# Kernel tuning notes

Measured on AMD Instinct MI355X. Metric: run time of the kernel, lower is better.

Reference implementation:

```python
import jax, jax.numpy as jnp
import numpy as np

H = 256; DS = 8; DC = 4; DI = 512; DTR = 16; NH = 4; EPS = 1e-5
B, N, F, E, S, LC = 8, 512, 32, 8192, 512, 8


def setup_inputs() -> dict:
    key = jax.random.key(0)
    ks = iter(jax.random.split(key, 64))
    def rn(shape, s=0.05):
        return jax.random.normal(next(ks), shape, jnp.float32) * s
    z = lambda *s: jnp.zeros(s, jnp.float32)
    inp = dict(
        node_features=jax.random.normal(next(ks), (B, N, F), jnp.float32),
        edge_index=jax.random.randint(next(ks), (B, 2, E), 0, N),
        W_init=rn((F, H)), b_init=z(H),
        gcn1_W=rn((H, H)), gcn1_b=z(H),
        gcn2_W=rn((H, H)), gcn2_b=z(H),
        in_proj_W=rn((H, 2 * DI)),
        conv_W=rn((DI, DC)), conv_b=z(DI),
        xproj_W=rn((DI, DTR + 2 * DS)),
        dt_W=rn((DTR, DI)), dt_b=z(DI),
        A_log=jnp.log(jnp.tile(jnp.arange(1, DS + 1, dtype=jnp.float32), (DI, 1))),
        Dp=jnp.ones((DI,), jnp.float32),
        out_W=rn((DI, H)),
        Wq=rn((H, H)), bq=z(H), Wk=rn((H, H)), bk=z(H), Wv=rn((H, H)), bv=z(H),
        Wo=rn((H, H)), bo=z(H),
        fus_W=rn((3 * H, H)), fus_b=z(H),
        ln_g=jnp.ones((H,), jnp.float32), ln_b=z(H),
        cw=rn((H, 1)), cb=z(1), hw=rn((H, 4)), hb=z(4), tw=rn((H, 3)), tb=z(3),
        p1w=rn((H, S)), p1b=z(S), p2w=rn((H, S)), p2b=z(S),
        dw=rn((H, S)), db=z(S), sw=rn((H, LC)), sb=z(LC))
    return inp


def gcn(x, src, dst, W, b):
    # PyG GCNConv: self-loops + symmetric deg^{-1/2} normalization, scatter-add.
    n = x.shape[0]
    loops = jnp.arange(n)
    s = jnp.concatenate([src, loops]); d = jnp.concatenate([dst, loops])
    deg = jax.ops.segment_sum(jnp.ones_like(d, x.dtype), d, n)
    dinv = jnp.where(deg > 0, jax.lax.rsqrt(deg), 0.0)
    norm = (dinv[s] * dinv[d])[:, None]
    m = x @ W
    return jax.ops.segment_sum(m[s] * norm, d, n) + b


def mamba(x, in_W, conv_W, conv_b, xproj_W, dt_W, dt_b, A_log, Dp, out_W):
    # mamba_ssm Mamba block, batch=1, seq len L = total nodes.
    L = x.shape[0]
    xz = x @ in_W
    xc, zg = xz[:, :DI], xz[:, DI:]
    xp = jnp.pad(xc, ((DC - 1, 0), (0, 0)))            # causal depthwise conv
    win = xp[jnp.arange(L)[:, None] + jnp.arange(DC)[None, :]]  # [L,K,DI]
    xc = jax.nn.silu(jnp.einsum('lkd,dk->ld', win, conv_W) + conv_b)
    proj = xc @ xproj_W
    dt, Bm, Cm = proj[:, :DTR], proj[:, DTR:DTR + DS], proj[:, DTR + DS:]
    delta = jax.nn.softplus(dt @ dt_W + dt_b)           # [L,DI]
    A = -jnp.exp(A_log)                                 # [DI,DS]
    dA = jnp.exp(delta[:, :, None] * A[None])           # [L,DI,DS]
    dBx = delta[:, :, None] * Bm[:, None, :] * xc[:, :, None]
    def step(h, inp):
        dA_t, dBx_t, C_t = inp
        h = dA_t * h + dBx_t
        return h, (h * C_t[None, :]).sum(-1)
    _, y = jax.lax.scan(step, jnp.zeros((DI, DS), x.dtype), (dA, dBx, Cm))
    y = (y + Dp * xc) * jax.nn.silu(zg)
    return y @ out_W


def mha(x, Wq, bq, Wk, bk, Wv, bv, Wo, bo):
    L = x.shape[0]; hd = H // NH
    q = (x @ Wq + bq).reshape(L, NH, hd)
    k = (x @ Wk + bk).reshape(L, NH, hd)
    v = (x @ Wv + bv).reshape(L, NH, hd)
    s = jnp.einsum('qhd,khd->hqk', q, k) / np.float32(np.sqrt(hd))
    a = jax.nn.softmax(s, axis=-1)
    o = jnp.einsum('hqk,khd->qhd', a, v).reshape(L, H)
    return o @ Wo + bo


def _forward(node_features, edge_index, W_init, b_init, gcn1_W, gcn1_b, gcn2_W, gcn2_b,
             in_proj_W, conv_W, conv_b, xproj_W, dt_W, dt_b, A_log, Dp, out_W,
             Wq, bq, Wk, bk, Wv, bv, Wo, bo, fus_W, fus_b, ln_g, ln_b,
             cw, cb, hw, hb, tw, tb, p1w, p1b, p2w, p2b, dw, db, sw, sb):
    Bsz, Nn, Ff = node_features.shape
    x = node_features.reshape(Bsz * Nn, Ff)
    # offset per-graph edge indices into the flat node space (batching loop)
    ei = (edge_index + (jnp.arange(Bsz) * Nn)[:, None, None]).transpose(1, 0, 2).reshape(2, -1)
    src, dst = ei[0], ei[1]
    h = jax.nn.relu(x @ W_init + b_init)
    h = jax.nn.relu(gcn(h, src, dst, gcn1_W, gcn1_b))
    h = jax.nn.relu(gcn(h, src, dst, gcn2_W, gcn2_b))
    m = mamba(h, in_proj_W, conv_W, conv_b, xproj_W, dt_W, dt_b, A_log, Dp, out_W)
    a = mha(h, Wq, bq, Wk, bk, Wv, bv, Wo, bo)
    fused = jax.nn.relu(jnp.concatenate([h, m, a], -1) @ fus_W + fus_b)
    res = fused + h
    mu = res.mean(-1, keepdims=True)
    var = ((res - mu) ** 2).mean(-1, keepdims=True)
    hf = (res - mu) * jax.lax.rsqrt(var + EPS) * ln_g + ln_b
    batch = jnp.repeat(jnp.arange(Bsz), Nn)
    pooled = jax.ops.segment_sum(hf, batch, Bsz) / jnp.float32(Nn)  # global_mean_pool
    outs = [pooled @ cw + cb, pooled @ hw + hb, pooled @ tw + tb,
            pooled @ p1w + p1b, pooled @ p2w + p2b, pooled @ dw + db,
            pooled @ sw + sb]
    return jnp.concatenate(outs, -1)  # [B, 1+4+3+S+S+S+LC]


def reference(node_features, edge_index, W_init, b_init, gcn1_W, gcn1_b, gcn2_W, gcn2_b,
              in_proj_W, conv_W, conv_b, xproj_W, dt_W, dt_b, A_log, Dp, out_W,
              Wq, bq, Wk, bk, Wv, bv, Wo, bo, fus_W, fus_b, ln_g, ln_b,
              cw, cb, hw, hb, tw, tb, p1w, p1b, p2w, p2b, dw, db, sw, sb):
    return _forward(node_features, edge_index, W_init, b_init, gcn1_W, gcn1_b, gcn2_W, gcn2_b,
                    in_proj_W, conv_W, conv_b, xproj_W, dt_W, dt_b, A_log, Dp, out_W,
                    Wq, bq, Wk, bk, Wv, bv, Wo, bo, fus_W, fus_b, ln_g, ln_b,
                    cw, cb, hw, hb, tw, tb, p1w, p1b, p2w, p2b, dw, db, sw, sb)
```

## Files before the change

kernel.cpp:

```cpp
#include <hip/hip_runtime.h>
#include <hip/hip_bf16.h>
#include <math.h>

typedef __hip_bfloat16 hbf;
typedef short bf16x8 __attribute__((ext_vector_type(8)));
typedef float f32x4 __attribute__((ext_vector_type(4)));

constexpr int NL  = 4096;
constexpr int HH  = 256;
constexpr int NE  = 8192;
constexpr int DIc = 512;
constexpr int DSc = 8;
constexpr int CLc = 16;
constexpr int NOUT = 12416;

constexpr size_t O_MBUF  = 0;
constexpr size_t O_QK    = 1048576;
constexpr size_t O_H2    = 2097152;
constexpr size_t O_CATB  = 3145728;
constexpr size_t O_XZB   = 4718592;
constexpr size_t O_XC    = 6815744;
constexpr size_t O_DELTA = 8912896;
constexpr size_t O_PROJ  = 11010048;
constexpr size_t O_HST   = 11141120;
constexpr size_t O_Y     = 12189696;
constexpr size_t O_POOL  = 13238272;
constexpr size_t O_DINV  = 13240320;
constexpr size_t O_B768  = 13244416;
constexpr size_t O_INT   = 13245184;
constexpr size_t O_WT    = 13327112;
constexpr size_t O_XB    = 13839112;
constexpr size_t O_H0B   = 13904648;
constexpr size_t O_H2B   = 14428936;
constexpr size_t O_XCB   = 14953224;
constexpr size_t O_DTAB  = 16001800;
constexpr size_t O_QKB   = 16067584;
constexpr size_t O_VTB   = 17116160;
constexpr size_t O_PART  = 17640448;
constexpr size_t O_HWT   = 17902592;

constexpr int NW = 12;
__device__ __constant__ int wc_cum[NW+1] = {
    0, 8192, 73728, 139264, 155648, 172032, 303104, 565248,
    630784, 696320, 761856, 827392, 1024000 };
__device__ __constant__ int wc_K [NW] = {32,256,256,512,16,512,256,256,256,256,256,768};
__device__ __constant__ int wc_N [NW] = {256,256,256,32,512,256,1024,256,256,256,256,256};
__device__ __constant__ int wc_Kp[NW] = {32,256,256,512,32,512,256,256,256,256,256,768};
struct WSrc { const float* p[NW]; };
struct HSrc { const float* p[7]; };
struct OPtrs { hbf* p[8]; };

__device__ __constant__ int hw_b[8]  = {0,1,5,8,520,1032,1544,1552};
__device__ __constant__ int hw_nc[7] = {1,4,3,512,512,512,8};

constexpr int PR_W = 1024000;
constexpr int PR_X = PR_W + 131072;
constexpr int PR_B = PR_X + 768;
constexpr int PR_P = PR_B + 262144;
constexpr int PR_I = PR_P + 4096;
constexpr int PR_H = PR_I + 397312;
__global__ __launch_bounds__(256) void prep_k(WSrc ws, hbf* __restrict__ wt,
        const float* __restrict__ x, hbf* __restrict__ xb,
        const float* __restrict__ bq, const float* __restrict__ bk,
        const float* __restrict__ bv,
        float* __restrict__ b768, float* __restrict__ part, int* __restrict__ cnt,
        HSrc hs, hbf* __restrict__ hwt) {
    int idx = blockIdx.x*256 + threadIdx.x;
    if (idx < PR_W) {
        int lo = 0, hi = NW-1;
        while (lo < hi) { int mid = (lo+hi+1)>>1; if (idx >= wc_cum[mid]) lo = mid; else hi = mid-1; }
        int local = idx - wc_cum[lo];
        int Kp = wc_Kp[lo], K = wc_K[lo], N = wc_N[lo];
        int n = local / Kp, k = local - n*Kp;
        float v = (k < K) ? ws.p[lo][(size_t)k*N + n] : 0.0f;
        wt[idx] = __float2bfloat16(v);
    } else if (idx < PR_X) {
        int i = idx - PR_W;
        xb[i] = __float2bfloat16(x[i]);
    } else if (idx < PR_B) {
        int i = idx - PR_X;
        b768[i] = (i < 256) ? bq[i] : (i < 512 ? bk[i-256] : bv[i-512]);
    } else if (idx < PR_P) {
        part[idx - PR_B] = 0.0f;
    } else if (idx < PR_I) {
        cnt[idx - PR_P] = 0;
    } else if (idx < PR_H) {
        int i = idx - PR_I;
        int j = i >> 8, k = i & 255;
        int seg = 0;
        while (j >= hw_b[seg+1]) seg++;
        int col = j - hw_b[seg], nc = hw_nc[seg];
        hwt[(size_t)j*256 + k] = __float2bfloat16(hs.p[seg][(size_t)k*nc + col]);
    }
}

__global__ void bucket_k(const int* __restrict__ ei, int* __restrict__ cnt,
                         int* __restrict__ csr) {
    int i = blockIdx.x*256 + threadIdx.x;
    int b = i >> 13, e = i & 8191;
    int src = ei[b*2*NE + e]      + (b << 9);
    int dst = ei[b*2*NE + NE + e] + (b << 9);
    int slot = atomicAdd(&cnt[dst], 1);
    if (slot < 64) csr[(dst << 6) + slot] = src;
}

__global__ __launch_bounds__(256) void gather_k(const hbf* __restrict__ m,
                        const int* __restrict__ csr, const int* __restrict__ cnt,
                        hbf* __restrict__ outb) {
    int n = blockIdx.x, c = threadIdx.x;
    int cn = min(cnt[n], 64);
    float dn = rsqrtf(1.0f + (float)cn);
    float acc = __bfloat162float(m[(size_t)n*HH + c]) * dn * dn;
    for (int e = 0; e < cn; e++) {
        int s = csr[(n << 6) + e];
        float ds = rsqrtf(1.0f + (float)min(cnt[s], 64));
        acc += __bfloat162float(m[(size_t)s*HH + c]) * (ds * dn);
    }
    outb[(size_t)n*HH + c] = __float2bfloat16(acc);
}

template<int ACT, int OUTM>
__global__ __launch_bounds__(512) void mg_k(const unsigned short* __restrict__ A,
        const unsigned short* __restrict__ Bt, const float* __restrict__ bias,
        void* __restrict__ Cp, int ldc, void* __restrict__ Cp2, void* __restrict__ Cp3,
        const float* __restrict__ resid, int ldr, int M, int K, int N)
{
    __shared__ __align__(16) unsigned short Asm[2][64][40];
    __shared__ __align__(16) unsigned short Bsm[2][64][40];
    int t = threadIdx.x;
    int lane = t & 63, w = t >> 6;
    int wm = w & 3, wn = w >> 2;
    int row0 = blockIdx.x * 64, col0 = blockIdx.y * 64;
    int sr = t >> 3;
    int sk8 = (t & 7) * 8;
    int su = sk8 >> 5, so = sk8 & 31;
    f32x4 acc0 = {}, acc1 = {};
    int fr = lane & 15, fq8 = (lane >> 4) * 8;

    uint4 zz = make_uint4(0u,0u,0u,0u);
    uint4 ra = zz, rb = zz;
    bool bnv = (col0 + sr) < N;
    if (sk8 < K) {
        ra = *(const uint4*)&A[(size_t)(row0+sr)*K + sk8];
        if (bnv) rb = *(const uint4*)&Bt[(size_t)(col0+sr)*K + sk8];
    }

    for (int k0 = 0; k0 < K; k0 += 64) {
        __syncthreads();
        *(uint4*)&Asm[su][sr][so] = ra;
        *(uint4*)&Bsm[su][sr][so] = rb;
        __syncthreads();
        int kn = k0 + 64;
        if (kn < K) {
            ra = rb = zz;
            if (kn + sk8 < K) {
                ra = *(const uint4*)&A[(size_t)(row0+sr)*K + kn + sk8];
                if (bnv) rb = *(const uint4*)&Bt[(size_t)(col0+sr)*K + kn + sk8];
            }
        }
        #pragma unroll
        for (int ks = 0; ks < 2; ks++) {
            bf16x8 a  = *(bf16x8*)&Asm[ks][wm*16 + fr][fq8];
            bf16x8 b0 = *(bf16x8*)&Bsm[ks][wn*32 + fr][fq8];
            bf16x8 b1 = *(bf16x8*)&Bsm[ks][wn*32 + 16 + fr][fq8];
            acc0 = __builtin_amdgcn_mfma_f32_16x16x32_bf16(a, b0, acc0, 0, 0, 0);
            acc1 = __builtin_amdgcn_mfma_f32_16x16x32_bf16(a, b1, acc1, 0, 0, 0);
        }
    }

    int fc = lane & 15, frq = (lane >> 4) * 4;
    if constexpr (OUTM == 4) {
        #pragma unroll
        for (int nt = 0; nt < 2; nt++) {
            int col = col0 + wn*32 + nt*16 + fc;
            if (col >= 32) continue;
            f32x4& av = nt ? acc1 : acc0;
            #pragma unroll
            for (int i = 0; i < 4; i++) {
                int row = row0 + wm*16 + frq + i;
                float v = av[i];
                ((float*)Cp)[(size_t)row*32 + col] = v;
                ((hbf*)Cp2)[(size_t)row*32 + col] = __float2bfloat16((col < 16) ? v : 0.0f);
            }
        }
    } else if constexpr (OUTM == 5) {
        if (col0 < 1024) {
            #pragma unroll
            for (int nt = 0; nt < 2; nt++) {
                int col = col0 + wn*32 + nt*16 + fc;
                f32x4& av = nt ? acc1 : acc0;
                #pragma unroll
                for (int i = 0; i < 4; i++) {
                    int row = row0 + wm*16 + frq + i;
                    ((hbf*)Cp)[(size_t)row*1024 + col] = __float2bfloat16(av[i]);
                }
            }
        } else if (col0 < 1536) {
            #pragma unroll
            for (int nt = 0; nt < 2; nt++) {
                int gcol = col0 + wn*32 + nt*16 + fc;
                int col = gcol - 1024;
                float bvv = bias[col];
                float sc = (col < 256) ? 0.125f : 1.0f;
                f32x4& av = nt ? acc1 : acc0;
                #pragma unroll
                for (int i = 0; i < 4; i++) {
                    int row = row0 + wm*16 + frq + i;
                    ((hbf*)Cp2)[(size_t)row*512 + col] = __float2bfloat16((av[i] + bvv) * sc);
                }
            }
        } else {
            __shared__ __align__(16) unsigned short Ts[64][72];
            #pragma unroll
            for (int nt = 0; nt < 2; nt++) {
                int gcol = col0 + wn*32 + nt*16 + fc;
                float bvv = bias[gcol - 1024];
                f32x4& av = nt ? acc1 : acc0;
                #pragma unroll
                for (int i = 0; i < 4; i++)
                    *(hbf*)&Ts[wn*32 + nt*16 + fc][wm*16 + frq + i] = __float2bfloat16(av[i] + bvv);
            }
            __syncthreads();
            int c = t >> 3, rs = (t & 7) * 8;
            *(uint4*)((hbf*)Cp3 + (size_t)(col0 - 1536 + c)*NL + row0 + rs) = *(uint4*)&Ts[c][rs];
        }
    } else if constexpr (OUTM == 6) {
        #pragma unroll
        for (int nt = 0; nt < 2; nt++) {
            int col = col0 + wn*32 + nt*16 + fc;
            float bvv = bias[col];
            f32x4& av = nt ? acc1 : acc0;
            #pragma unroll
            for (int i = 0; i < 4; i++) {
                int row = row0 + wm*16 + frq + i;
                float v = fmaxf(av[i] + bvv, 0.0f);
                ((float*)Cp)[(size_t)row*HH + col] = v;
                hbf hv = __float2bfloat16(v);
                ((hbf*)Cp2)[(size_t)row*HH + col] = hv;
                ((hbf*)Cp3)[(size_t)row*768 + col] = hv;
            }
        }
    } else {
        #pragma unroll
        for (int nt = 0; nt < 2; nt++) {
            int col = col0 + wn*32 + nt*16 + fc;
            if (col >= N) continue;
            float bvv = bias ? bias[col] : 0.0f;
            f32x4& av = nt ? acc1 : acc0;
            #pragma unroll
            for (int i = 0; i < 4; i++) {
                int row = row0 + wm*16 + frq + i;
                float v = av[i] + bvv;
                if (ACT == 1) v = fmaxf(v, 0.0f);
                if (ACT == 2) v = (v > 20.0f) ? v : log1pf(expf(v));
                if (resid) v += resid[(size_t)row*ldr + col];
                if (OUTM == 0) ((float*)Cp)[(size_t)row*ldc + col] = v;
                else           ((hbf*)Cp)[(size_t)row*ldc + col] = __float2bfloat16(v);
            }
        }
    }
}

__global__ __launch_bounds__(256) void conv_k(const hbf* __restrict__ xzb,
                       const float* __restrict__ cW,
                       const float* __restrict__ cb, hbf* __restrict__ xcb) {
    int i = blockIdx.x*256 + threadIdx.x;
    int l = i >> 6, d8 = (i & 63) << 3;
    float acc[8];
    {
        float4 c0 = *(const float4*)&cb[d8];
        float4 c1 = *(const float4*)&cb[d8+4];
        acc[0]=c0.x; acc[1]=c0.y; acc[2]=c0.z; acc[3]=c0.w;
        acc[4]=c1.x; acc[5]=c1.y; acc[6]=c1.z; acc[7]=c1.w;
    }
    float4 cw4[8];
    #pragma unroll
    for (int j = 0; j < 8; j++) cw4[j] = *(const float4*)&cW[(d8+j)*4];
    #pragma unroll
    for (int k = 0; k < 4; k++) {
        int ls = l - 3 + k;
        if (ls < 0) continue;
        bf16x8 v = *(const bf16x8*)&xzb[(size_t)ls*1024 + d8];
        #pragma unroll
        for (int j = 0; j < 8; j++) {
            short tv = v[j]; hbf hv; *(short*)&hv = tv;
            float wk = (k == 0) ? cw4[j].x : (k == 1) ? cw4[j].y : (k == 2) ? cw4[j].z : cw4[j].w;
            acc[j] += __bfloat162float(hv) * wk;
        }
    }
    hbf out[8];
    #pragma unroll
    for (int j = 0; j < 8; j++) {
        float r = acc[j] / (1.0f + __expf(-acc[j]));
        out[j] = __float2bfloat16(r);
    }
    *(uint4*)&xcb[(size_t)l*512 + d8] = *(uint4*)out;
}

__global__ __launch_bounds__(256) void scan1_k(const float* __restrict__ delta,
                        const hbf* __restrict__ xc, const float* __restrict__ proj,
                        const float* __restrict__ Alog,
                        float* __restrict__ P, float* __restrict__ Hl)
{
    int c = blockIdx.x >> 1;
    int d = ((blockIdx.x & 1) << 8) + threadIdx.x;
    float Ac[DSc], pr[DSc], h[DSc];
    #pragma unroll
    for (int s2 = 0; s2 < DSc; s2++) { Ac[s2] = -__expf(Alog[d*DSc+s2]); pr[s2]=1.0f; h[s2]=0.0f; }
    int l0 = c * CLc;
    for (int l = l0; l < l0 + CLc; l++) {
        float dl = delta[(size_t)l*DIc + d];
        float dx = dl * __bfloat162float(xc[(size_t)l*DIc + d]);
        const float* pb = proj + l*32 + 16;
        #pragma unroll
        for (int s2 = 0; s2 < DSc; s2++) {
            float a = __expf(dl * Ac[s2]);
            h[s2] = a*h[s2] + dx*pb[s2];
            pr[s2] *= a;
        }
    }
    #pragma unroll
    for (int s2 = 0; s2 < DSc; s2++) {
        P [(size_t)(c*DSc+s2)*DIc + d] = pr[s2];
        Hl[(size_t)(c*DSc+s2)*DIc + d] = h[s2];
    }
}

__global__ __launch_bounds__(256) void scan2t_k(const float* __restrict__ P,
                        const float* __restrict__ Hl, float* __restrict__ Hst) {
    __shared__ float Ps[256][17], Hs[256][17];
    int t = threadIdx.x, sg = blockIdx.x;
    int si = t & 15, cb = t >> 4;
    #pragma unroll
    for (int it = 0; it < 16; it++) {
        int c = it*16 + cb;
        size_t off = (size_t)c*4096 + sg*16 + si;
        Ps[c][si] = P[off];
        Hs[c][si] = Hl[off];
    }
    __syncthreads();
    int si2 = t >> 4, g = t & 15;
    int lane = t & 63;
    float Pg = 1.0f, Hg = 0.0f;
    #pragma unroll
    for (int j = 0; j < 16; j++) {
        int c = g*16 + j;
        float pc = Ps[c][si2], hc = Hs[c][si2];
        Hg = hc + pc*Hg;
        Pg = pc*Pg;
    }
    #pragma unroll
    for (int off = 1; off < 16; off <<= 1) {
        float Pp = __shfl(Pg, lane - off);
        float Hp = __shfl(Hg, lane - off);
        if (g >= off) { Hg = Hg + Pg*Hp; Pg = Pg*Pp; }
    }
    float carry = __shfl(Hg, lane - 1);
    if (g == 0) carry = 0.0f;
    float h = carry;
    #pragma unroll
    for (int j = 0; j < 16; j++) {
        int c = g*16 + j;
        float pc = Ps[c][si2], hc = Hs[c][si2];
        Hs[c][si2] = h;
        h = hc + pc*h;
    }
    __syncthreads();
    #pragma unroll
    for (int it = 0; it < 16; it++) {
        int c = it*16 + cb;
        Hst[(size_t)c*4096 + sg*16 + si] = Hs[c][si];
    }
}

__global__ __launch_bounds__(256) void scan3_k(const float* __restrict__ delta,
                        const hbf* __restrict__ xc, const float* __restrict__ proj,
                        const float* __restrict__ Alog, const float* __restrict__ Hst,
                        const float* __restrict__ Dp, const hbf* __restrict__ xzb,
                        hbf* __restrict__ Y)
{
    int c = blockIdx.x >> 1;
    int d = ((blockIdx.x & 1) << 8) + threadIdx.x;
    float Ac[DSc], h[DSc];
    #pragma unroll
    for (int s2 = 0; s2 < DSc; s2++) {
        Ac[s2] = -__expf(Alog[d*DSc+s2]);
        h[s2]  = Hst[(size_t)(c*DSc+s2)*DIc + d];
    }
    float dpv = Dp[d];
    int l0 = c * CLc;
    for (int l = l0; l < l0 + CLc; l++) {
        float dl = delta[(size_t)l*DIc + d];
        float xv = __bfloat162float(xc[(size_t)l*DIc + d]);
        float dx = dl * xv;
        const float* pb = proj + l*32 + 16;
        float y = 0.0f;
        #pragma unroll
        for (int s2 = 0; s2 < DSc; s2++) {
            float a = __expf(dl * Ac[s2]);
            h[s2] = a*h[s2] + dx*pb[s2];
            y += h[s2] * pb[8+s2];
        }
        float z = __bfloat162float(xzb[(size_t)l*1024 + 512 + d]);
        float sz = z / (1.0f + __expf(-z));
        Y[(size_t)l*DIc + d] = __float2bfloat16((y + dpv*xv) * sz);
    }
}

__global__ __launch_bounds__(512, 8) void attn_part_k(const unsigned short* __restrict__ QK,
                       const unsigned short* __restrict__ Vt,
                       OPtrs op, float* __restrict__ lsum)
{
    __shared__ __align__(16) unsigned short QPs[128][72];
    __shared__ __align__(16) unsigned short Ks[64][72];
    __shared__ __align__(16) unsigned short Vs[64][72];
    int t = threadIdx.x, lane = t & 63, w = t >> 6;
    int h = blockIdx.y, q0 = blockIdx.x * 128, skc = blockIdx.z;
    int fm = lane & 15, fq = lane >> 4;

    {
        int qr = t >> 2, qc = (t & 3) * 16;
        const unsigned short* src = &QK[(size_t)(q0+qr)*512 + h*64 + qc];
        *(uint4*)&QPs[qr][qc]     = *(const uint4*)&src[0];
        *(uint4*)&QPs[qr][qc + 8] = *(const uint4*)&src[8];
    }
    __syncthreads();
    bf16x8 qa[2];
    #pragma unroll
    for (int ks = 0; ks < 2; ks++)
        qa[ks] = *(bf16x8*)&QPs[w*16 + fm][ks*32 + fq*8];

    bf16x8 ones;
    #pragma unroll
    for (int j = 0; j < 8; j++) ones[j] = (short)0x3F80;

    f32x4 o[4] = {};
    f32x4 ol = {};
    int sr = t >> 3, sk = (t & 7) * 8;
    const unsigned short* Kb = QK + 256;
    int kt = skc * 512;
    uint4 ka = *(const uint4*)&Kb[(size_t)(kt+sr)*512 + h*64 + sk];
    uint4 va = *(const uint4*)&Vt[(size_t)(h*64+sr)*NL + kt + sk];

    for (int it = 0; it < 8; it++) {
        __syncthreads();
        *(uint4*)&Ks[sr][sk] = ka;
        *(uint4*)&Vs[sr][sk] = va;
        __syncthreads();
        if (it < 7) {
            int kn = kt + 64;
            ka = *(const uint4*)&Kb[(size_t)(kn+sr)*512 + h*64 + sk];
            va = *(const uint4*)&Vt[(size_t)(h*64+sr)*NL + kn + sk];
        }
        #pragma unroll
        for (int np = 0; np < 2; np++) {
            f32x4 s0 = {}, s1 = {};
            __builtin_amdgcn_s_setprio(1);
            #pragma unroll
            for (int ks = 0; ks < 2; ks++) {
                bf16x8 kb0 = *(bf16x8*)&Ks[(np*2+0)*16 + fm][ks*32 + fq*8];
                bf16x8 kb1 = *(bf16x8*)&Ks[(np*2+1)*16 + fm][ks*32 + fq*8];
                s0 = __builtin_amdgcn_mfma_f32_16x16x32_bf16(qa[ks], kb0, s0, 0, 0, 0);
                s1 = __builtin_amdgcn_mfma_f32_16x16x32_bf16(qa[ks], kb1, s1, 0, 0, 0);
            }
            __builtin_amdgcn_s_setprio(0);
            #pragma unroll
            for (int i = 0; i < 4; i++) {
                float p0 = __expf(s0[i] - 4.0f);
                float p1 = __expf(s1[i] - 4.0f);
                *(hbf*)&QPs[w*16 + fq*4 + i][(np*2+0)*16 + fm] = __float2bfloat16(p0);
                *(hbf*)&QPs[w*16 + fq*4 + i][(np*2+1)*16 + fm] = __float2bfloat16(p1);
            }
        }
        __builtin_amdgcn_s_setprio(1);
        #pragma unroll
        for (int ks = 0; ks < 2; ks++) {
            bf16x8 pa = *(bf16x8*)&QPs[w*16 + fm][ks*32 + fq*8];
            #pragma unroll
            for (int nt = 0; nt < 4; nt++) {
                bf16x8 vb = *(bf16x8*)&Vs[nt*16 + fm][ks*32 + fq*8];
                o[nt] = __builtin_amdgcn_mfma_f32_16x16x32_bf16(pa, vb, o[nt], 0, 0, 0);
            }
            ol = __builtin_amdgcn_mfma_f32_16x16x32_bf16(pa, ones, ol, 0, 0, 0);
        }
        __builtin_amdgcn_s_setprio(0);
        kt += 64;
    }
    hbf* Op = op.p[skc];
    #pragma unroll
    for (int i = 0; i < 4; i++) {
        int row = w*16 + fq*4 + i;
        #pragma unroll
        for (int nt = 0; nt < 4; nt++)
            Op[(size_t)(q0 + row)*HH + h*64 + nt*16 + fm] = __float2bfloat16(o[nt][i]);
    }
    if (fm == 0) {
        #pragma unroll
        for (int i = 0; i < 4; i++)
            lsum[(size_t)(skc*4 + h)*NL + q0 + w*16 + fq*4 + i] = ol[i];
    }
}

__global__ __launch_bounds__(256) void amerge_k(OPtrs op, const float* __restrict__ lsum,
                                                hbf* __restrict__ aob) {
    int row = blockIdx.x, t = threadIdx.x, h = t >> 6;
    float L = 0.0f, s = 0.0f;
    #pragma unroll
    for (int c = 0; c < 8; c++) {
        L += lsum[(size_t)(c*4 + h)*NL + row];
        s += __bfloat162float(op.p[c][(size_t)row*HH + t]);
    }
    aob[(size_t)row*HH + t] = __float2bfloat16(s / L);
}

__global__ __launch_bounds__(256) void ln_k(const float* __restrict__ X,
                    const float* __restrict__ g, const float* __restrict__ b,
                    float* __restrict__ part) {
    __shared__ float red[4];
    int r = blockIdx.x, t = threadIdx.x;
    float v = X[(size_t)r*HH + t];
    float s = v;
    #pragma unroll
    for (int o = 32; o > 0; o >>= 1) s += __shfl_down(s, o);
    if ((t & 63) == 0) red[t >> 6] = s;
    __syncthreads();
    float mean = (red[0]+red[1]+red[2]+red[3]) * (1.0f/256.0f);
    float dfv = v - mean;
    float s2 = dfv*dfv;
    #pragma unroll
    for (int o = 32; o > 0; o >>= 1) s2 += __shfl_down(s2, o);
    __syncthreads();
    if ((t & 63) == 0) red[t >> 6] = s2;
    __syncthreads();
    float var = (red[0]+red[1]+red[2]+red[3]) * (1.0f/256.0f);
    float y = dfv * rsqrtf(var + 1e-5f) * g[t] + b[t];
    atomicAdd(&part[(size_t)(r & 127)*2048 + (r >> 9)*HH + t], y * (1.0f/512.0f));
}

__global__ void reduce_k(const float* __restrict__ part, float* __restrict__ pooled) {
    int i = blockIdx.x*256 + threadIdx.x;
    float s = 0.0f;
    #pragma unroll 8
    for (int p = 0; p < 128; p++) s += part[(size_t)p*2048 + i];
    pooled[i] = s;
}

__global__ __launch_bounds__(256) void heads_k(const float* __restrict__ pooled,
        const hbf* __restrict__ hwt,
        const float* cbh, const float* hb, const float* tb, const float* p1b,
        const float* p2b, const float* db, const float* sb, float* __restrict__ out)
{
    int idx = blockIdx.x*4 + (threadIdx.x >> 6);
    int lane = threadIdx.x & 63;
    if (idx >= NOUT) return;
    int b = idx / 1552, j = idx - b*1552;
    const float* bi; int col;
    if (j < 1)         { bi = cbh; col = j;        }
    else if (j < 5)    { bi = hb;  col = j - 1;    }
    else if (j < 8)    { bi = tb;  col = j - 5;    }
    else if (j < 520)  { bi = p1b; col = j - 8;    }
    else if (j < 1032) { bi = p2b; col = j - 520;  }
    else if (j < 1544) { bi = db;  col = j - 1032; }
    else               { bi = sb;  col = j - 1544; }
    const float* pl = pooled + b*HH;
    const hbf* wr = hwt + (size_t)j*256;
    int k4 = lane * 4;
    float4 pv = *(const float4*)&pl[k4];
    short4 wv = *(const short4*)&wr[k4];
    hbf w0, w1, w2, w3;
    *(short*)&w0 = wv.x; *(short*)&w1 = wv.y; *(short*)&w2 = wv.z; *(short*)&w3 = wv.w;
    float s = pv.x*__bfloat162float(w0) + pv.y*__bfloat162float(w1)
            + pv.z*__bfloat162float(w2) + pv.w*__bfloat162float(w3);
    #pragma unroll
    for (int o = 32; o > 0; o >>= 1) s += __shfl_down(s, o);
    if (lane == 0) out[idx] = s + bi[col];
}

extern "C" void kernel_launch(void* const* d_in, const int* in_sizes, int n_in,
                              void* d_out, int out_size, void* d_ws, size_t ws_size,
                              hipStream_t stream)
{
    (void)in_sizes; (void)n_in; (void)out_size; (void)ws_size;
    const float* x      = (const float*)d_in[0];
    const int*   ei     = (const int*)  d_in[1];
    const float* W_init = (const float*)d_in[2];
    const float* b_init = (const float*)d_in[3];
    const float* g1W = (const float*)d_in[4];
    const float* g1b = (const float*)d_in[5];
    const float* g2W = (const float*)d_in[6];
    const float* g2b = (const float*)d_in[7];
    const float* inW = (const float*)d_in[8];
    const float* cW  = (const float*)d_in[9];
    const float* cb  = (const float*)d_in[10];
    const float* xpW = (const float*)d_in[11];
    const float* dtW = (const float*)d_in[12];
    const float* dtb = (const float*)d_in[13];
    const float* Alog= (const float*)d_in[14];
    const float* Dp  = (const float*)d_in[15];
    const float* outW= (const float*)d_in[16];
    const float* Wq  = (const float*)d_in[17];
    const float* bq  = (const float*)d_in[18];
    const float* Wk  = (const float*)d_in[19];
    const float* bk  = (const float*)d_in[20];
    const float* Wv  = (const float*)d_in[21];
    const float* bv  = (const float*)d_in[22];
    const float* Wo  = (const float*)d_in[23];
    const float* bo  = (const float*)d_in[24];
    const float* fusW= (const float*)d_in[25];
    const float* fusb= (const float*)d_in[26];
    const float* lng = (const float*)d_in[27];
    const float* lnb = (const float*)d_in[28];
    const float* cwp = (const float*)d_in[29];
    const float* cbp = (const float*)d_in[30];
    const float* hwp = (const float*)d_in[31];
    const float* hbp = (const float*)d_in[32];
    const float* twp = (const float*)d_in[33];
    const float* tbp = (const float*)d_in[34];
    const float* p1w = (const float*)d_in[35];
    const float* p1b = (const float*)d_in[36];
    const float* p2w = (const float*)d_in[37];
    const float* p2b = (const float*)d_in[38];
    const float* dwp = (const float*)d_in[39];
    const float* dbp = (const float*)d_in[40];
    const float* swp = (const float*)d_in[41];
    const float* sbp = (const float*)d_in[42];

    float* fw = (float*)d_ws;
    int* iw = (int*)(fw + O_INT);
    int* cnt = iw;
    int* csr = (int*)(fw + O_XC);

    hbf* wt   = (hbf*)(fw + O_WT);
    hbf* xb   = (hbf*)(fw + O_XB);
    hbf* h0b  = (hbf*)(fw + O_H0B);
    hbf* h2b  = (hbf*)(fw + O_H2B);
    hbf* xcb  = (hbf*)(fw + O_XCB);
    hbf* dtab = (hbf*)(fw + O_DTAB);
    hbf* xzb  = (hbf*)(fw + O_XZB);
    hbf* yb   = (hbf*)(fw + O_Y);
    hbf* aob  = (hbf*)(fw + O_Y);
    hbf* catb = (hbf*)(fw + O_CATB);
    hbf* qkB  = (hbf*)(fw + O_QKB);
    hbf* vtB  = (hbf*)(fw + O_VTB);
    hbf* aggb = (hbf*)(fw + O_MBUF);
    float* fused = fw + O_XC;
    float* b768 = fw + O_B768;
    float* part = fw + O_PART;
    hbf* hwt  = (hbf*)(fw + O_HWT);

    float* scanP  = fw + O_MBUF;
    float* scanHl = fw + O_QK;
    float* scanHst= fw + O_HST;
    float* lsum   = fw + O_HST;

    OPtrs op;
    op.p[0] = (hbf*)(fw + O_MBUF);
    op.p[1] = (hbf*)(fw + O_MBUF + 524288);
    op.p[2] = (hbf*)(fw + O_DELTA);
    op.p[3] = (hbf*)(fw + O_DELTA + 524288);
    op.p[4] = (hbf*)(fw + O_DELTA + 1048576);
    op.p[5] = (hbf*)(fw + O_DELTA + 1572864);
    op.p[6] = (hbf*)(fw + O_XZB);
    op.p[7] = (hbf*)(fw + O_XZB + 524288);

    hbf* WtInit  = wt + 0;
    hbf* WtG1    = wt + 8192;
    hbf* WtG2    = wt + 73728;
    hbf* WtXp    = wt + 139264;
    hbf* WtDt    = wt + 155648;
    hbf* WtOut   = wt + 172032;
    hbf* WtInQKV = wt + 303104;
    hbf* WtO     = wt + 761856;
    hbf* WtFus   = wt + 827392;

    WSrc wsrc;
    wsrc.p[0]=W_init; wsrc.p[1]=g1W; wsrc.p[2]=g2W; wsrc.p[3]=xpW; wsrc.p[4]=dtW;
    wsrc.p[5]=outW; wsrc.p[6]=inW; wsrc.p[7]=Wq; wsrc.p[8]=Wk; wsrc.p[9]=Wv;
    wsrc.p[10]=Wo; wsrc.p[11]=fusW;
    HSrc hsrc;
    hsrc.p[0]=cwp; hsrc.p[1]=hwp; hsrc.p[2]=twp; hsrc.p[3]=p1w;
    hsrc.p[4]=p2w; hsrc.p[5]=dwp; hsrc.p[6]=swp;
    prep_k<<<(PR_H+255)/256,256,0,stream>>>(wsrc, wt, x, xb, bq, bk, bv, b768,
                                            part, cnt, hsrc, hwt);

    bucket_k<<<256,256,0,stream>>>(ei, cnt, csr);

    mg_k<1,1><<<dim3(64,4),512,0,stream>>>((const unsigned short*)xb, (const unsigned short*)WtInit,
        b_init, h0b, 256, nullptr, nullptr, nullptr, 0, NL, 32, 256);
    gather_k<<<4096,256,0,stream>>>(h0b, csr, cnt, aggb);
    mg_k<1,1><<<dim3(64,4),512,0,stream>>>((const unsigned short*)aggb, (const unsigned short*)WtG1,
        g1b, h0b, 256, nullptr, nullptr, nullptr, 0, NL, 256, 256);
    gather_k<<<4096,256,0,stream>>>(h0b, csr, cnt, aggb);
    mg_k<1,6><<<dim3(64,4),512,0,stream>>>((const unsigned short*)aggb, (const unsigned short*)WtG2,
        g2b, fw+O_H2, 256, h2b, catb, nullptr, 0, NL, 256, 256);

    mg_k<0,5><<<dim3(64,28),512,0,stream>>>((const unsigned short*)h2b, (const unsigned short*)WtInQKV,
        b768, xzb, 1024, qkB, vtB, nullptr, 0, NL, 256, 1792);

    conv_k<<<1024,256,0,stream>>>(xzb, cW, cb, xcb);
    mg_k<0,4><<<dim3(64,1),512,0,stream>>>((const unsigned short*)xcb, (const unsigned short*)WtXp,
        nullptr, fw+O_PROJ, 32, dtab, nullptr, nullptr, 0, NL, 512, 32);
    mg_k<2,0><<<dim3(64,8),512,0,stream>>>((const unsigned short*)dtab, (const unsigned short*)WtDt,
        dtb, fw+O_DELTA, 512, nullptr, nullptr, nullptr, 0, NL, 32, 512);
    scan1_k<<<512,256,0,stream>>>(fw+O_DELTA, xcb, fw+O_PROJ, Alog, scanP, scanHl);
    scan2t_k<<<256,256,0,stream>>>(scanP, scanHl, scanHst);
    scan3_k<<<512,256,0,stream>>>(fw+O_DELTA, xcb, fw+O_PROJ, Alog, scanHst, Dp, xzb, yb);
    mg_k<0,1><<<dim3(64,4),512,0,stream>>>((const unsigned short*)yb, (const unsigned short*)WtOut,
        nullptr, catb + 256, 768, nullptr, nullptr, nullptr, 0, NL, 512, 256);

    attn_part_k<<<dim3(32,4,8),512,0,stream>>>((const unsigned short*)qkB,
        (const unsigned short*)vtB, op, lsum);
    amerge_k<<<4096,256,0,stream>>>(op, lsum, aob);
    mg_k<0,1><<<dim3(64,4),512,0,stream>>>((const unsigned short*)aob, (const unsigned short*)WtO,
        bo, catb + 512, 768, nullptr, nullptr, nullptr, 0, NL, 256, 256);

    mg_k<1,0><<<dim3(64,4),512,0,stream>>>((const unsigned short*)catb, (const unsigned short*)WtFus,
        fusb, fused, 256, nullptr, nullptr, fw+O_H2, 256, NL, 768, 256);
    ln_k<<<4096,256,0,stream>>>(fused, lng, lnb, part);
    reduce_k<<<8,256,0,stream>>>(part, fw+O_POOL);
    heads_k<<<(NOUT+3)/4,256,0,stream>>>(fw+O_POOL, hwt, cbp,hbp,tbp,p1b,p2b,dbp,sbp,
                                         (float*)d_out);
}
```

Before: 352.5 us.

## Shrink GEMM tiles to 32x32 for more blocks; vectorize attention merge

The bf16 MFMA GEMM kernel moves from 64x64 tiles with 512 threads to 32x32 tiles with 256 threads, so each wave computes a single 16x16 tile. Every GEMM launch gets four times as many blocks, which fills more of the GPU's compute units for these small M=4096 problems. In exchange, each block reuses loaded data less and the B-column bounds check is dropped. The attention merge kernel now has each thread handle 8 contiguous bf16 values with vector loads and stores, 8 rows per block, instead of one element per thread.

```diff
diff --git a/kernel.cpp b/kernel.cpp
--- a/kernel.cpp
+++ b/kernel.cpp
@@ -120,137 +120,110 @@
 }
 
 template<int ACT, int OUTM>
-__global__ __launch_bounds__(512) void mg_k(const unsigned short* __restrict__ A,
+__global__ __launch_bounds__(256) void mg_k(const unsigned short* __restrict__ A,
         const unsigned short* __restrict__ Bt, const float* __restrict__ bias,
         void* __restrict__ Cp, int ldc, void* __restrict__ Cp2, void* __restrict__ Cp3,
         const float* __restrict__ resid, int ldr, int M, int K, int N)
 {
-    __shared__ __align__(16) unsigned short Asm[2][64][40];
-    __shared__ __align__(16) unsigned short Bsm[2][64][40];
+    __shared__ __align__(16) unsigned short Asm[2][32][40];
+    __shared__ __align__(16) unsigned short Bsm[2][32][40];
     int t = threadIdx.x;
     int lane = t & 63, w = t >> 6;
-    int wm = w & 3, wn = w >> 2;
-    int row0 = blockIdx.x * 64, col0 = blockIdx.y * 64;
-    int sr = t >> 3;
-    int sk8 = (t & 7) * 8;
-    int su = sk8 >> 5, so = sk8 & 31;
-    f32x4 acc0 = {}, acc1 = {};
+    int wr = (w & 1) * 16, wc = (w >> 1) * 16;
+    int row0 = blockIdx.x * 32, col0 = blockIdx.y * 32;
+    int sr = t >> 3, sk8 = (t & 7) * 8;
+    f32x4 acc = {};
     int fr = lane & 15, fq8 = (lane >> 4) * 8;
 
     uint4 zz = make_uint4(0u,0u,0u,0u);
     uint4 ra = zz, rb = zz;
-    bool bnv = (col0 + sr) < N;
     if (sk8 < K) {
         ra = *(const uint4*)&A[(size_t)(row0+sr)*K + sk8];
-        if (bnv) rb = *(const uint4*)&Bt[(size_t)(col0+sr)*K + sk8];
+        rb = *(const uint4*)&Bt[(size_t)(col0+sr)*K + sk8];
     }
 
     for (int k0 = 0; k0 < K; k0 += 64) {
         __syncthreads();
-        *(uint4*)&Asm[su][sr][so] = ra;
-        *(uint4*)&Bsm[su][sr][so] = rb;
+        *(uint4*)&Asm[sk8>>5][sr][sk8 & 31] = ra;
+        *(uint4*)&Bsm[sk8>>5][sr][sk8 & 31] = rb;
         __syncthreads();
         int kn = k0 + 64;
         if (kn < K) {
             ra = rb = zz;
             if (kn + sk8 < K) {
                 ra = *(const uint4*)&A[(size_t)(row0+sr)*K + kn + sk8];
-                if (bnv) rb = *(const uint4*)&Bt[(size_t)(col0+sr)*K + kn + sk8];
+                rb = *(const uint4*)&Bt[(size_t)(col0+sr)*K + kn + sk8];
             }
         }
         #pragma unroll
         for (int ks = 0; ks < 2; ks++) {
-            bf16x8 a  = *(bf16x8*)&Asm[ks][wm*16 + fr][fq8];
-            bf16x8 b0 = *(bf16x8*)&Bsm[ks][wn*32 + fr][fq8];
-            bf16x8 b1 = *(bf16x8*)&Bsm[ks][wn*32 + 16 + fr][fq8];
-            acc0 = __builtin_amdgcn_mfma_f32_16x16x32_bf16(a, b0, acc0, 0, 0, 0);
-            acc1 = __builtin_amdgcn_mfma_f32_16x16x32_bf16(a, b1, acc1, 0, 0, 0);
+            bf16x8 a = *(bf16x8*)&Asm[ks][wr + fr][fq8];
+            bf16x8 b = *(bf16x8*)&Bsm[ks][wc + fr][fq8];
+            acc = __builtin_amdgcn_mfma_f32_16x16x32_bf16(a, b, acc, 0, 0, 0);
         }
     }
 
     int fc = lane & 15, frq = (lane >> 4) * 4;
     if constexpr (OUTM == 4) {
-        #pragma unroll
-        for (int nt = 0; nt < 2; nt++) {
-            int col = col0 + wn*32 + nt*16 + fc;
-            if (col >= 32) continue;
-            f32x4& av = nt ? acc1 : acc0;
+        int col = wc + fc;
+        #pragma unroll
+        for (int i = 0; i < 4; i++) {
+            int row = row0 + wr + frq + i;
+            float v = acc[i];
+            ((float*)Cp)[(size_t)row*32 + col] = v;
+            ((hbf*)Cp2)[(size_t)row*32 + col] = __float2bfloat16((col < 16) ? v : 0.0f);
+        }
+    } else if constexpr (OUTM == 5) {
+        if (col0 < 1024) {
+            int col = col0 + wc + fc;
             #pragma unroll
             for (int i = 0; i < 4; i++) {
-                int row = row0 + wm*16 + frq + i;
-                float v = av[i];
-                ((float*)Cp)[(size_t)row*32 + col] = v;
-                ((hbf*)Cp2)[(size_t)row*32 + col] = __float2bfloat16((col < 16) ? v : 0.0f);
-            }
-        }
-    } else if constexpr (OUTM == 5) {
-        if (col0 < 1024) {
-            #pragma unroll
-            for (int nt = 0; nt < 2; nt++) {
-                int col = col0 + wn*32 + nt*16 + fc;
-                f32x4& av = nt ? acc1 : acc0;
-                #pragma unroll
-                for (int i = 0; i < 4; i++) {
-                    int row = row0 + wm*16 + frq + i;
-                    ((hbf*)Cp)[(size_t)row*1024 + col] = __float2bfloat16(av[i]);
-                }
+                int row = row0 + wr + frq + i;
+                ((hbf*)Cp)[(size_t)row*1024 + col] = __float2bfloat16(acc[i]);
             }
         } else if (col0 < 1536) {
+            int gcol = col0 + wc + fc;
+            int col = gcol - 1024;
+            float bvv = bias[col];
+            float sc = (col < 256) ? 0.125f : 1.0f;
             #pragma unroll
-            for (int nt = 0; nt < 2; nt++) {
-                int gcol = col0 + wn*32 + nt*16 + fc;
-                int col = gcol - 1024;
-                float bvv = bias[col];
-                float sc = (col < 256) ? 0.125f : 1.0f;
-                f32x4& av = nt ? acc1 : acc0;
-                #pragma unroll
-                for (int i = 0; i < 4; i++) {
-                    int row = row0 + wm*16 + frq + i;
-                    ((hbf*)Cp2)[(size_t)row*512 + col] = __float2bfloat16((av[i] + bvv) * sc);
-                }
+            for (int i = 0; i < 4; i++) {
+                int row = row0 + wr + frq + i;
+                ((hbf*)Cp2)[(size_t)row*512 + col] = __float2bfloat16((acc[i] + bvv) * sc);
             }
         } else {
-            __shared__ __align__(16) unsigned short Ts[64][72];
+            __shared__ __align__(16) unsigned short Ts[32][48];
+            int gcol = col0 + wc + fc;
+            float bvv = bias[gcol - 1024];
             #pragma unroll
-            for (int nt = 0; nt < 2; nt++) {
-                int gcol = col0 + wn*32 + nt*16 + fc;
-                float bvv = bias[gcol - 1024];
-                f32x4& av = nt ? acc1 : acc0;
-                #pragma unroll
-                for (int i = 0; i < 4; i++)
-                    *(hbf*)&Ts[wn*32 + nt*16 + fc][wm*16 + frq + i] = __float2bfloat16(av[i] + bvv);
+            for (int i = 0; i < 4; i++)
+                *(hbf*)&Ts[wc + fc][wr + frq + i] = __float2bfloat16(acc[i] + bvv);
+            __syncthreads();
+            if (t < 128) {
+                int c = t >> 2, rs = (t & 3) * 8;
+                *(uint4*)((hbf*)Cp3 + (size_t)(col0 - 1536 + c)*NL + row0 + rs) = *(uint4*)&Ts[c][rs];
             }
-            __syncthreads();
-            int c = t >> 3, rs = (t & 7) * 8;
-            *(uint4*)((hbf*)Cp3 + (size_t)(col0 - 1536 + c)*NL + row0 + rs) = *(uint4*)&Ts[c][rs];
         }
     } else if constexpr (OUTM == 6) {
-        #pragma unroll
-        for (int nt = 0; nt < 2; nt++) {
-            int col = col0 + wn*32 + nt*16 + fc;
-            float bvv = bias[col];
-            f32x4& av = nt ? acc1 : acc0;
+        int col = col0 + wc + fc;
+        float bvv = bias[col];
+        #pragma unroll
+        for (int i = 0; i < 4; i++) {
+            int row = row0 + wr + frq + i;
+            float v = fmaxf(acc[i] + bvv, 0.0f);
+            ((float*)Cp)[(size_t)row*HH + col] = v;
+            hbf hv = __float2bfloat16(v);
+            ((hbf*)Cp2)[(size_t)row*HH + col] = hv;
+            ((hbf*)Cp3)[(size_t)row*768 + col] = hv;
+        }
+    } else {
+        int col = col0 + wc + fc;
+        if (col < N) {
+            float bvv = bias ? bias[col] : 0.0f;
             #pragma unroll
             for (int i = 0; i < 4; i++) {
-                int row = row0 + wm*16 + frq + i;
-                float v = fmaxf(av[i] + bvv, 0.0f);
-                ((float*)Cp)[(size_t)row*HH + col] = v;
-                hbf hv = __float2bfloat16(v);
-                ((hbf*)Cp2)[(size_t)row*HH + col] = hv;
-                ((hbf*)Cp3)[(size_t)row*768 + col] = hv;
-            }
-        }
-    } else {
-        #pragma unroll
-        for (int nt = 0; nt < 2; nt++) {
-            int col = col0 + wn*32 + nt*16 + fc;
-            if (col >= N) continue;
-            float bvv = bias ? bias[col] : 0.0f;
-            f32x4& av = nt ? acc1 : acc0;
-            #pragma unroll
-            for (int i = 0; i < 4; i++) {
-                int row = row0 + wm*16 + frq + i;
-                float v = av[i] + bvv;
+                int row = row0 + wr + frq + i;
+                float v = acc[i] + bvv;
                 if (ACT == 1) v = fmaxf(v, 0.0f);
                 if (ACT == 2) v = (v > 20.0f) ? v : log1pf(expf(v));
                 if (resid) v += resid[(size_t)row*ldr + col];
@@ -503,14 +476,28 @@
 
 __global__ __launch_bounds__(256) void amerge_k(OPtrs op, const float* __restrict__ lsum,
                                                 hbf* __restrict__ aob) {
-    int row = blockIdx.x, t = threadIdx.x, h = t >> 6;
-    float L = 0.0f, s = 0.0f;
+    int t = threadIdx.x;
+    int row = blockIdx.x*8 + (t >> 5);
+    int d8 = (t & 31) << 3;
+    int h = d8 >> 6;
+    float L = 0.0f;
+    #pragma unroll
+    for (int c = 0; c < 8; c++) L += lsum[(size_t)(c*4 + h)*NL + row];
+    float inv = 1.0f / L;
+    float s[8] = {};
     #pragma unroll
     for (int c = 0; c < 8; c++) {
-        L += lsum[(size_t)(c*4 + h)*NL + row];
-        s += __bfloat162float(op.p[c][(size_t)row*HH + t]);
-    }
-    aob[(size_t)row*HH + t] = __float2bfloat16(s / L);
+        bf16x8 v = *(const bf16x8*)&op.p[c][(size_t)row*HH + d8];
+        #pragma unroll
+        for (int j = 0; j < 8; j++) {
+            short tv = v[j]; hbf hv; *(short*)&hv = tv;
+            s[j] += __bfloat162float(hv);
+        }
+    }
+    hbf out[8];
+    #pragma unroll
+    for (int j = 0; j < 8; j++) out[j] = __float2bfloat16(s[j] * inv);
+    *(uint4*)&aob[(size_t)row*HH + d8] = *(uint4*)out;
 }
 
 __global__ __launch_bounds__(256) void ln_k(const float* __restrict__ X,
@@ -685,36 +672,36 @@
 
     bucket_k<<<256,256,0,stream>>>(ei, cnt, csr);
 
-    mg_k<1,1><<<dim3(64,4),512,0,stream>>>((const unsigned short*)xb, (const unsigned short*)WtInit,
+    mg_k<1,1><<<dim3(128,8),256,0,stream>>>((const unsigned short*)xb, (const unsigned short*)WtInit,
         b_init, h0b, 256, nullptr, nullptr, nullptr, 0, NL, 32, 256);
     gather_k<<<4096,256,0,stream>>>(h0b, csr, cnt, aggb);
-    mg_k<1,1><<<dim3(64,4),512,0,stream>>>((const unsigned short*)aggb, (const unsigned short*)WtG1,
+    mg_k<1,1><<<dim3(128,8),256,0,stream>>>((const unsigned short*)aggb, (const unsigned short*)WtG1,
         g1b, h0b, 256, nullptr, nullptr, nullptr, 0, NL, 256, 256);
     gather_k<<<4096,256,0,stream>>>(h0b, csr, cnt, aggb);
-    mg_k<1,6><<<dim3(64,4),512,0,stream>>>((const unsigned short*)aggb, (const unsigned short*)WtG2,
+    mg_k<1,6><<<dim3(128,8),256,0,stream>>>((const unsigned short*)aggb, (const unsigned short*)WtG2,
         g2b, fw+O_H2, 256, h2b, catb, nullptr, 0, NL, 256, 256);
 
-    mg_k<0,5><<<dim3(64,28),512,0,stream>>>((const unsigned short*)h2b, (const unsigned short*)WtInQKV,
+    mg_k<0,5><<<dim3(128,56),256,0,stream>>>((const unsigned short*)h2b, (const unsigned short*)WtInQKV,
         b768, xzb, 1024, qkB, vtB, nullptr, 0, NL, 256, 1792);
 
     conv_k<<<1024,256,0,stream>>>(xzb, cW, cb, xcb);
-    mg_k<0,4><<<dim3(64,1),512,0,stream>>>((const unsigned short*)xcb, (const unsigned short*)WtXp,
+    mg_k<0,4><<<dim3(128,1),256,0,stream>>>((const unsigned short*)xcb, (const unsigned short*)WtXp,
         nullptr, fw+O_PROJ, 32, dtab, nullptr, nullptr, 0, NL, 512, 32);
-    mg_k<2,0><<<dim3(64,8),512,0,stream>>>((const unsigned short*)dtab, (const unsigned short*)WtDt,
+    mg_k<2,0><<<dim3(128,16),256,0,stream>>>((const unsigned short*)dtab, (const unsigned short*)WtDt,
         dtb, fw+O_DELTA, 512, nullptr, nullptr, nullptr, 0, NL, 32, 512);
     scan1_k<<<512,256,0,stream>>>(fw+O_DELTA, xcb, fw+O_PROJ, Alog, scanP, scanHl);
     scan2t_k<<<256,256,0,stream>>>(scanP, scanHl, scanHst);
     scan3_k<<<512,256,0,stream>>>(fw+O_DELTA, xcb, fw+O_PROJ, Alog, scanHst, Dp, xzb, yb);
-    mg_k<0,1><<<dim3(64,4),512,0,stream>>>((const unsigned short*)yb, (const unsigned short*)WtOut,
+    mg_k<0,1><<<dim3(128,8),256,0,stream>>>((const unsigned short*)yb, (const unsigned short*)WtOut,
         nullptr, catb + 256, 768, nullptr, nullptr, nullptr, 0, NL, 512, 256);
 
     attn_part_k<<<dim3(32,4,8),512,0,stream>>>((const unsigned short*)qkB,
         (const unsigned short*)vtB, op, lsum);
-    amerge_k<<<4096,256,0,stream>>>(op, lsum, aob);
-    mg_k<0,1><<<dim3(64,4),512,0,stream>>>((const unsigned short*)aob, (const unsigned short*)WtO,
+    amerge_k<<<512,256,0,stream>>>(op, lsum, aob);
+    mg_k<0,1><<<dim3(128,8),256,0,stream>>>((const unsigned short*)aob, (const unsigned short*)WtO,
         bo, catb + 512, 768, nullptr, nullptr, nullptr, 0, NL, 256, 256);
 
-    mg_k<1,0><<<dim3(64,4),512,0,stream>>>((const unsigned short*)catb, (const unsigned short*)WtFus,
+    mg_k<1,0><<<dim3(128,8),256,0,stream>>>((const unsigned short*)catb, (const unsigned short*)WtFus,
         fusb, fused, 256, nullptr, nullptr, fw+O_H2, 256, NL, 768, 256);
     ln_k<<<4096,256,0,stream>>>(fused, lng, lnb, part);
     reduce_k<<<8,256,0,stream>>>(part, fw+O_POOL);
```

After: 342.0 us. 1.03x faster.
